# Kernel optimization log

Hardware: AMD Instinct MI355X
Metric: run time of the kernel (lower is better)

Reference implementation:

```python
import jax, jax.numpy as jnp
import numpy as np

B, S, D, H = 2, 2048, 1024, 16
DK = D // H  # 64


def setup_inputs() -> dict:
    key = jax.random.key(0)
    ks = jax.random.split(key, 11)
    std = 1.0 / np.sqrt(D)
    inp = {
        "q": jax.random.normal(ks[0], (B, S, D), jnp.float32),
        "k": jax.random.normal(ks[1], (B, S, D), jnp.float32),
        "v": jax.random.normal(ks[2], (B, S, D), jnp.float32),
        # causal mask: True means masked (matches masked_fill(mask == True, -1e9))
        "mask": jnp.triu(jnp.ones((1, 1, S, S), dtype=bool), k=1),
        "Wq": jax.random.normal(ks[3], (D, D), jnp.float32) * std,
        "bq": jnp.zeros((D,), jnp.float32),
        "Wk": jax.random.normal(ks[4], (D, D), jnp.float32) * std,
        "bk": jnp.zeros((D,), jnp.float32),
        "Wv": jax.random.normal(ks[5], (D, D), jnp.float32) * std,
        "bv": jnp.zeros((D,), jnp.float32),
        "Wo": jax.random.normal(ks[6], (D, D), jnp.float32) * std,
        "bo": jnp.zeros((D,), jnp.float32),
    }
    return inp


def _split_heads(x):
    b, s, _ = x.shape
    return x.reshape(b, s, H, DK).transpose(0, 2, 1, 3)  # [B,H,S,DK]


def reference(q, k, v, mask, Wq, bq, Wk, bk, Wv, bv, Wo, bo):
    # QKV projections (nn.Linear: x @ W.T + b)
    qh = _split_heads(q @ Wq.T + bq)
    kh = _split_heads(k @ Wk.T + bk)
    vh = _split_heads(v @ Wv.T + bv)
    # scaled dot-product attention (dropout is identity in eval)
    scores = jnp.einsum("bhqd,bhkd->bhqk", qh, kh) / jnp.sqrt(
        jnp.asarray(DK, jnp.float32))
    scores = jnp.where(mask, jnp.float32(-1e9), scores)
    attn = jax.nn.softmax(scores, axis=-1)
    out = jnp.einsum("bhqk,bhkd->bhqd", attn, vh)
    # combine heads [B,H,S,DK] -> [B,S,D], then output projection
    out = out.transpose(0, 2, 1, 3).reshape(q.shape[0], -1, D)
    return out @ Wo.T + bo
```

## Files before the change

### kernel.cpp

```cpp
#include <hip/hip_runtime.h>
#include <stdint.h>

#define S_LEN 2048
#define DMODEL 1024
#define NHEAD 16
#define DKH 64

typedef __attribute__((ext_vector_type(8))) short short8;
typedef __attribute__((ext_vector_type(4))) short sv4;
typedef __attribute__((ext_vector_type(4))) float fv4;
typedef __attribute__((ext_vector_type(8))) __bf16 bf16x8;
typedef __attribute__((ext_vector_type(4))) float f32x4;

#define QSCALE 0.18033688011112042f

static __device__ __forceinline__ short f2bf(float f) {
  unsigned u = __builtin_bit_cast(unsigned, f);
  u = u + 0x7fffu + ((u >> 16) & 1u);
  return (short)(u >> 16);
}

static __device__ __forceinline__ bf16x8 ldfrag(const void* p) {
  return __builtin_bit_cast(bf16x8, *(const short8*)p);
}

#define GLL16(gp, lp) __builtin_amdgcn_global_load_lds( \
    (const __attribute__((address_space(1))) unsigned int*)(const void*)(gp), \
    (__attribute__((address_space(3))) unsigned int*)(void*)(lp), 16, 0, 0)

#define WAIT_VMCNT0() asm volatile("s_waitcnt vmcnt(0)" ::: "memory")
#define WAIT_LGKM0()  asm volatile("s_waitcnt lgkmcnt(0)" ::: "memory")

__global__ __launch_bounds__(256) void convert_all(
    const float* __restrict__ q, const float* __restrict__ k, const float* __restrict__ v,
    const float* __restrict__ wq, const float* __restrict__ wk, const float* __restrict__ wv,
    const float* __restrict__ wo,
    short* __restrict__ xb, short* __restrict__ wb, short* __restrict__ wob)
{
  const int total = 4194304;
  for (int gid = blockIdx.x * blockDim.x + threadIdx.x; gid < total;
       gid += gridDim.x * blockDim.x) {
    const float* src; short* dst; int off; float scl = 1.0f;
    if (gid < 3145728) {
      int z = gid >> 20;
      off = (gid & 1048575) << 2;
      src = (z == 0) ? q : (z == 1) ? k : v;
      dst = xb + (size_t)z * 4194304;
    } else {
      int g = gid - 3145728;
      int z = g >> 18;
      off = (g & 262143) << 2;
      src = (z == 0) ? wq : (z == 1) ? wk : (z == 2) ? wv : wo;
      dst = (z < 3) ? (wb + (size_t)z * 1048576) : wob;
      if (z == 0) scl = QSCALE;
    }
    fv4 f = *(const fv4*)(src + off);
    sv4 o;
    o.x = f2bf(f.x * scl); o.y = f2bf(f.y * scl);
    o.z = f2bf(f.z * scl); o.w = f2bf(f.w * scl);
    *(sv4*)(dst + off) = o;
  }
}

__global__ __launch_bounds__(256) void gemm_proj(
    const short* __restrict__ Abase, const short* __restrict__ Wbase,
    const float* __restrict__ bias0, const float* __restrict__ bias1,
    const float* __restrict__ bias2, float bscl0,
    short* __restrict__ Cbf)
{
  const int Kd = 1024, Nd = 1024, Md = 4096;
  const int z = blockIdx.z;
  const short* A = Abase + (size_t)z * Md * Kd;
  const short* W = Wbase + (size_t)z * Nd * Kd;
  const float* bias = (z == 0) ? bias0 : (z == 1) ? bias1 : bias2;
  const float bscl = (z == 0) ? bscl0 : 1.0f;

  __shared__ short8 AB[2048];
  short8* As = AB;
  short8* Bs = AB + 1024;

  const int tid = threadIdx.x;
  const int w = tid >> 6, lane = tid & 63;
  const int wr = w >> 1, wc = w & 1;
  const int lhi = lane >> 4, llo = lane & 15;
  const int id = blockIdx.x + 8 * blockIdx.y;
  const int sw = (id & 7) * 32 + (id >> 3);
  const int n0 = (sw & 7) * 128, m0 = (sw >> 3) * 128;

  const f32x4 zero = {0.f, 0.f, 0.f, 0.f};
  f32x4 acc[4][4];
#pragma unroll
  for (int i = 0; i < 4; ++i)
#pragma unroll
    for (int j = 0; j < 4; ++j) acc[i][j] = zero;

  for (int kt = 0; kt < Kd / 64; ++kt) {
    const int k0 = kt * 64;
    __syncthreads();
#pragma unroll
    for (int inst = 0; inst < 4; ++inst) {
      int ib = w * 4096 + inst * 1024 + lane * 16;
      int row = ib >> 7;
      int colb = (ib & 127) ^ ((row & 7) << 4);
      int col = colb >> 1;
      GLL16(A + (size_t)(m0 + row) * Kd + k0 + col,
            (char*)As + (w * 4096 + inst * 1024));
      GLL16(W + (size_t)(n0 + row) * Kd + k0 + col,
            (char*)Bs + (w * 4096 + inst * 1024));
    }
    __syncthreads();
#pragma unroll
    for (int kk = 0; kk < 2; ++kk) {
      bf16x8 af[4], bfm[4];
#pragma unroll
      for (int t = 0; t < 4; ++t) {
        int arow = wr * 64 + t * 16 + llo;
        int abyte = ((arow << 7) + ((kk * 32 + lhi * 8) << 1)) ^ ((arow & 7) << 4);
        af[t] = ldfrag((const char*)As + abyte);
        int brow = wc * 64 + t * 16 + llo;
        int bbyte = ((brow << 7) + ((kk * 32 + lhi * 8) << 1)) ^ ((brow & 7) << 4);
        bfm[t] = ldfrag((const char*)Bs + bbyte);
      }
#pragma unroll
      for (int i = 0; i < 4; ++i)
#pragma unroll
        for (int j = 0; j < 4; ++j)
          acc[i][j] = __builtin_amdgcn_mfma_f32_16x16x32_bf16(af[i], bfm[j], acc[i][j], 0, 0, 0);
    }
  }

  short* Co = Cbf + (size_t)z * Md * Nd;
  __syncthreads();
  short* Cs = (short*)AB;
#pragma unroll
  for (int i = 0; i < 4; ++i) {
#pragma unroll
    for (int j = 0; j < 4; ++j) {
      int col = wc * 64 + j * 16 + llo;
      float bv_ = bias[n0 + col] * bscl;
#pragma unroll
      for (int r = 0; r < 4; ++r) {
        int row = wr * 64 + i * 16 + lhi * 4 + r;
        Cs[row * 128 + col] = f2bf(acc[i][j][r] + bv_);
      }
    }
  }
  __syncthreads();
#pragma unroll
  for (int s = 0; s < 8; ++s) {
    int lb = s * 4096 + tid * 16;
    short8 vL = *(const short8*)((const char*)Cs + lb);
    int row = lb >> 8;
    int colb = lb & 255;
    *(short8*)&Co[(size_t)(m0 + row) * Nd + n0 + (colb >> 1)] = vL;
  }
}

__global__ __launch_bounds__(256) void gemm_out(
    const short* __restrict__ A, const short* __restrict__ W,
    const float* __restrict__ bias, float* __restrict__ Cf)
{
  const int Kd = 1024, Nd = 1024;

  __shared__ short8 As[1024];
  __shared__ short8 Bs[512];

  const int tid = threadIdx.x;
  const int w = tid >> 6, lane = tid & 63;
  const int wr = w >> 1, wc = w & 1;
  const int lhi = lane >> 4, llo = lane & 15;
  const int id = blockIdx.x + 16 * blockIdx.y;
  const int sw = (id & 7) * 64 + (id >> 3);
  const int n0 = (sw & 15) * 64, m0 = (sw >> 4) * 128;

  const f32x4 zero = {0.f, 0.f, 0.f, 0.f};
  f32x4 acc[4][2];
#pragma unroll
  for (int i = 0; i < 4; ++i)
#pragma unroll
    for (int j = 0; j < 2; ++j) acc[i][j] = zero;

  for (int kt = 0; kt < Kd / 64; ++kt) {
    const int k0 = kt * 64;
    __syncthreads();
#pragma unroll
    for (int inst = 0; inst < 4; ++inst) {
      int ib = w * 4096 + inst * 1024 + lane * 16;
      int row = ib >> 7;
      int colb = (ib & 127) ^ ((row & 7) << 4);
      GLL16(A + (size_t)(m0 + row) * Kd + k0 + (colb >> 1),
            (char*)As + (w * 4096 + inst * 1024));
    }
#pragma unroll
    for (int inst = 0; inst < 2; ++inst) {
      int ib = w * 2048 + inst * 1024 + lane * 16;
      int row = ib >> 7;
      int colb = (ib & 127) ^ ((row & 7) << 4);
      GLL16(W + (size_t)(n0 + row) * Kd + k0 + (colb >> 1),
            (char*)Bs + (w * 2048 + inst * 1024));
    }
    __syncthreads();
#pragma unroll
    for (int kk = 0; kk < 2; ++kk) {
      bf16x8 af[4], bfm[2];
#pragma unroll
      for (int t = 0; t < 4; ++t) {
        int arow = wr * 64 + t * 16 + llo;
        int abyte = ((arow << 7) + ((kk * 32 + lhi * 8) << 1)) ^ ((arow & 7) << 4);
        af[t] = ldfrag((const char*)As + abyte);
      }
#pragma unroll
      for (int j = 0; j < 2; ++j) {
        int brow = wc * 32 + j * 16 + llo;
        int bbyte = ((brow << 7) + ((kk * 32 + lhi * 8) << 1)) ^ ((brow & 7) << 4);
        bfm[j] = ldfrag((const char*)Bs + bbyte);
      }
#pragma unroll
      for (int i = 0; i < 4; ++i)
#pragma unroll
        for (int j = 0; j < 2; ++j)
          acc[i][j] = __builtin_amdgcn_mfma_f32_16x16x32_bf16(af[i], bfm[j], acc[i][j], 0, 0, 0);
    }
  }

#pragma unroll
  for (int i = 0; i < 4; ++i) {
#pragma unroll
    for (int j = 0; j < 2; ++j) {
      int col = n0 + wc * 32 + j * 16 + llo;
      float bv_ = bias[col];
#pragma unroll
      for (int r = 0; r < 4; ++r) {
        int row = m0 + wr * 64 + i * 16 + lhi * 4 + r;
        Cf[(size_t)row * Nd + col] = acc[i][j][r] + bv_;
      }
    }
  }
}

__global__ __launch_bounds__(256) void attn_fwd(
    const short* __restrict__ Qp, const short* __restrict__ Kp,
    const short* __restrict__ Vp, short* __restrict__ Out)
{
  __shared__ short8 Ks[2][512];
  __shared__ short  Vt[64 * 72];
  __shared__ short  PsA[4][16 * 72];

  const int tid = threadIdx.x;
  const int w = tid >> 6, lane = tid & 63;
  const int lhi = lane >> 4, llo = lane & 15;

  const int id = blockIdx.x;
  const int g  = id & 255;
  const int kq = id >> 8;
  const int wv = g & 7;
  const int bh = g >> 3;
  const int qt = (kq == 0) ? 2 * wv : (kq == 1) ? 31 - 2 * wv
               : (kq == 2) ? 2 * wv + 1 : 30 - 2 * wv;
  const int nt = qt + 1;
  const int qbase = qt * 64;
  const int b = bh >> 4, h = bh & 15;
  const size_t rowbase = (size_t)b * S_LEN;
  const short* Kbase = Kp + rowbase * DMODEL + h * DKH;
  const short* Vbase = Vp + rowbase * DMODEL + h * DKH;

  short* Ps = PsA[w];
  const f32x4 zero = {0.f, 0.f, 0.f, 0.f};

  bf16x8 qf[2];
  {
    const short* qrow = Qp + (rowbase + qbase + w * 16 + llo) * DMODEL + h * DKH;
    qf[0] = ldfrag(qrow + lhi * 8);
    qf[1] = ldfrag(qrow + 32 + lhi * 8);
  }

  float mr[4], lr[4];
  f32x4 oacc[4];
#pragma unroll
  for (int r = 0; r < 4; ++r) { mr[r] = -3.0e38f; lr[r] = 0.f; }
#pragma unroll
  for (int dt = 0; dt < 4; ++dt) oacc[dt] = zero;

  const int kvs = lane, dgrp = w;

#pragma unroll
  for (int inst = 0; inst < 2; ++inst) {
    int ib = w * 2048 + inst * 1024 + lane * 16;
    int row = ib >> 7;
    int colb = (ib & 127) ^ ((row & 7) << 4);
    GLL16(Kbase + (size_t)row * DMODEL + (colb >> 1),
          (char*)&Ks[0][0] + (w * 2048 + inst * 1024));
  }
  short8 va, vb;
  va = *(const short8*)(Vbase + (size_t)kvs * DMODEL + dgrp * 16);
  vb = *(const short8*)(Vbase + (size_t)kvs * DMODEL + dgrp * 16 + 8);

  for (int t = 0; t < nt; ++t) {
    const int cur = t & 1, nxt = cur ^ 1;
    const int kvbase = t * 64;

    WAIT_VMCNT0();
#pragma unroll
    for (int j = 0; j < 8; ++j) Vt[(dgrp * 16 + j) * 72 + kvs] = va[j];
#pragma unroll
    for (int j = 0; j < 8; ++j) Vt[(dgrp * 16 + 8 + j) * 72 + kvs] = vb[j];
    if (t + 1 < nt) {
      const int nb = kvbase + 64;
#pragma unroll
      for (int inst = 0; inst < 2; ++inst) {
        int ib = w * 2048 + inst * 1024 + lane * 16;
        int row = ib >> 7;
        int colb = (ib & 127) ^ ((row & 7) << 4);
        GLL16(Kbase + (size_t)(nb + row) * DMODEL + (colb >> 1),
              (char*)&Ks[nxt][0] + (w * 2048 + inst * 1024));
      }
      va = *(const short8*)(Vbase + (size_t)(nb + kvs) * DMODEL + dgrp * 16);
      vb = *(const short8*)(Vbase + (size_t)(nb + kvs) * DMODEL + dgrp * 16 + 8);
    }
    WAIT_LGKM0();
    __builtin_amdgcn_s_barrier();

    f32x4 sc[4];
#pragma unroll
    for (int tt = 0; tt < 4; ++tt) sc[tt] = zero;
    __builtin_amdgcn_s_setprio(1);
#pragma unroll
    for (int kk = 0; kk < 2; ++kk) {
#pragma unroll
      for (int tt = 0; tt < 4; ++tt) {
        int krow = tt * 16 + llo;
        int kbyte = ((krow << 7) + ((kk * 32 + lhi * 8) << 1)) ^ ((krow & 7) << 4);
        bf16x8 kf = ldfrag((const char*)&Ks[cur][0] + kbyte);
        sc[tt] = __builtin_amdgcn_mfma_f32_16x16x32_bf16(qf[kk], kf, sc[tt], 0, 0, 0);
      }
    }
    __builtin_amdgcn_s_setprio(0);

    const bool diag = (t == qt);
    float sv[4][4], tmx[4];
#pragma unroll
    for (int r = 0; r < 4; ++r) {
#pragma unroll
      for (int tt = 0; tt < 4; ++tt) {
        float s = sc[tt][r];
        if (diag) {
          int kg = kvbase + tt * 16 + llo;
          int qg = qbase + w * 16 + lhi * 4 + r;
          if (kg > qg) s = -3.0e38f;
        }
        sv[tt][r] = s;
      }
      float trm = fmaxf(fmaxf(sv[0][r], sv[1][r]), fmaxf(sv[2][r], sv[3][r]));
      trm = fmaxf(trm, __shfl_xor(trm, 1));
      trm = fmaxf(trm, __shfl_xor(trm, 2));
      trm = fmaxf(trm, __shfl_xor(trm, 4));
      trm = fmaxf(trm, __shfl_xor(trm, 8));
      tmx[r] = trm;
    }
    bool grow = (tmx[0] > mr[0] + 8.f) || (tmx[1] > mr[1] + 8.f) ||
                (tmx[2] > mr[2] + 8.f) || (tmx[3] > mr[3] + 8.f);
    if (__ballot(grow)) {
#pragma unroll
      for (int r = 0; r < 4; ++r) {
        float mnew = fmaxf(mr[r], tmx[r]);
        float alpha = __builtin_amdgcn_exp2f(mr[r] - mnew);
        mr[r] = mnew;
        lr[r] *= alpha;
#pragma unroll
        for (int dt = 0; dt < 4; ++dt) oacc[dt][r] = oacc[dt][r] * alpha;
      }
    }
#pragma unroll
    for (int r = 0; r < 4; ++r) {
      float rs = 0.f;
#pragma unroll
      for (int tt = 0; tt < 4; ++tt) {
        float pv = __builtin_amdgcn_exp2f(sv[tt][r] - mr[r]);
        rs += pv;
        Ps[(lhi * 4 + r) * 72 + tt * 16 + llo] = f2bf(pv);
      }
      lr[r] += rs;
    }

    __builtin_amdgcn_s_setprio(1);
#pragma unroll
    for (int kk = 0; kk < 2; ++kk) {
      bf16x8 pa = ldfrag(Ps + llo * 72 + kk * 32 + lhi * 8);
#pragma unroll
      for (int dt = 0; dt < 4; ++dt) {
        bf16x8 vf = ldfrag(&Vt[(dt * 16 + llo) * 72 + kk * 32 + lhi * 8]);
        oacc[dt] = __builtin_amdgcn_mfma_f32_16x16x32_bf16(pa, vf, oacc[dt], 0, 0, 0);
      }
    }
    __builtin_amdgcn_s_setprio(0);
    __builtin_amdgcn_s_barrier();
  }

#pragma unroll
  for (int r = 0; r < 4; ++r) {
    float rs = lr[r];
    rs += __shfl_xor(rs, 1);
    rs += __shfl_xor(rs, 2);
    rs += __shfl_xor(rs, 4);
    rs += __shfl_xor(rs, 8);
    lr[r] = rs;
  }
#pragma unroll
  for (int dt = 0; dt < 4; ++dt) {
#pragma unroll
    for (int r = 0; r < 4; ++r) {
      float vv = oacc[dt][r] / lr[r];
      int row = qbase + w * 16 + lhi * 4 + r;
      int col = h * DKH + dt * 16 + llo;
      Out[(rowbase + row) * DMODEL + col] = f2bf(vv);
    }
  }
}

extern "C" void kernel_launch(void* const* d_in, const int* in_sizes, int n_in,
                              void* d_out, int out_size, void* d_ws, size_t ws_size,
                              hipStream_t stream) {
  (void)in_sizes; (void)n_in; (void)out_size; (void)ws_size;
  const float* q  = (const float*)d_in[0];
  const float* k  = (const float*)d_in[1];
  const float* v  = (const float*)d_in[2];
  const float* Wq = (const float*)d_in[4];
  const float* bq = (const float*)d_in[5];
  const float* Wk = (const float*)d_in[6];
  const float* bk = (const float*)d_in[7];
  const float* Wv = (const float*)d_in[8];
  const float* bv = (const float*)d_in[9];
  const float* Wo = (const float*)d_in[10];
  const float* bo = (const float*)d_in[11];
  float* out = (float*)d_out;

  short* xb   = (short*)d_ws;
  short* wb   = xb + 3ull * 4194304;
  short* wob  = wb + 3ull * 1048576;
  short* proj = wob + 1048576;
  short* attno = xb;

  convert_all<<<dim3(2048), dim3(256), 0, stream>>>(q, k, v, Wq, Wk, Wv, Wo, xb, wb, wob);
  gemm_proj<<<dim3(8, 32, 3), dim3(256), 0, stream>>>(xb, wb, bq, bk, bv, QSCALE, proj);
  attn_fwd<<<dim3(1024), dim3(256), 0, stream>>>(proj, proj + 4194304ull,
                                                 proj + 2ull * 4194304, attno);
  gemm_out<<<dim3(16, 32), dim3(256), 0, stream>>>(attno, wob, bo, out);
}
```

Baseline: 256.4 us.

## Double-buffer GEMM LDS tiles and widen attention blocks to 128 query rows

Both projection GEMMs now stage the next K-tile into a second LDS buffer with global_load_lds before computing on the current one. Partial vmcnt waits and s_barrier replace the two __syncthreads per iteration, so loads overlap the MFMA work at the cost of doubled LDS use. The attention kernel moves to 512-thread blocks covering 128 query rows (8 waves), which halves the grid and shares each K/V tile between twice as many query rows. This adds per-block work imbalance and a wider diagonal-masking range.

New measurement: 257.3 us. Within noise of the previous version (+0.3%).

```diff
diff --git a/kernel.cpp b/kernel.cpp
--- a/kernel.cpp
+++ b/kernel.cpp
@@ -28,7 +28,7 @@
     (const __attribute__((address_space(1))) unsigned int*)(const void*)(gp), \
     (__attribute__((address_space(3))) unsigned int*)(void*)(lp), 16, 0, 0)
 
-#define WAIT_VMCNT0() asm volatile("s_waitcnt vmcnt(0)" ::: "memory")
+#define WAIT_VMCNT(N) asm volatile("s_waitcnt vmcnt(" #N ")" ::: "memory")
 #define WAIT_LGKM0()  asm volatile("s_waitcnt lgkmcnt(0)" ::: "memory")
 
 __global__ __launch_bounds__(256) void convert_all(
@@ -75,9 +75,7 @@
   const float* bias = (z == 0) ? bias0 : (z == 1) ? bias1 : bias2;
   const float bscl = (z == 0) ? bscl0 : 1.0f;
 
-  __shared__ short8 AB[2048];
-  short8* As = AB;
-  short8* Bs = AB + 1024;
+  __shared__ short8 AB[4096];
 
   const int tid = threadIdx.x;
   const int w = tid >> 6, lane = tid & 63;
@@ -94,9 +92,7 @@
 #pragma unroll
     for (int j = 0; j < 4; ++j) acc[i][j] = zero;
 
-  for (int kt = 0; kt < Kd / 64; ++kt) {
-    const int k0 = kt * 64;
-    __syncthreads();
+  auto stage = [&](int buf, int k0) {
 #pragma unroll
     for (int inst = 0; inst < 4; ++inst) {
       int ib = w * 4096 + inst * 1024 + lane * 16;
@@ -104,11 +100,24 @@
       int colb = (ib & 127) ^ ((row & 7) << 4);
       int col = colb >> 1;
       GLL16(A + (size_t)(m0 + row) * Kd + k0 + col,
-            (char*)As + (w * 4096 + inst * 1024));
+            (char*)AB + buf * 32768 + (w * 4096 + inst * 1024));
       GLL16(W + (size_t)(n0 + row) * Kd + k0 + col,
-            (char*)Bs + (w * 4096 + inst * 1024));
-    }
-    __syncthreads();
+            (char*)AB + buf * 32768 + 16384 + (w * 4096 + inst * 1024));
+    }
+  };
+
+  stage(0, 0);
+  for (int kt = 0; kt < 16; ++kt) {
+    const int cur = kt & 1, nxt = cur ^ 1;
+    if (kt < 15) {
+      stage(nxt, (kt + 1) * 64);
+      WAIT_VMCNT(8);
+    } else {
+      WAIT_VMCNT(0);
+    }
+    __builtin_amdgcn_s_barrier();
+    const char* As = (const char*)AB + cur * 32768;
+    const char* Bs = As + 16384;
 #pragma unroll
     for (int kk = 0; kk < 2; ++kk) {
       bf16x8 af[4], bfm[4];
@@ -116,10 +125,10 @@
       for (int t = 0; t < 4; ++t) {
         int arow = wr * 64 + t * 16 + llo;
         int abyte = ((arow << 7) + ((kk * 32 + lhi * 8) << 1)) ^ ((arow & 7) << 4);
-        af[t] = ldfrag((const char*)As + abyte);
+        af[t] = ldfrag(As + abyte);
         int brow = wc * 64 + t * 16 + llo;
         int bbyte = ((brow << 7) + ((kk * 32 + lhi * 8) << 1)) ^ ((brow & 7) << 4);
-        bfm[t] = ldfrag((const char*)Bs + bbyte);
+        bfm[t] = ldfrag(Bs + bbyte);
       }
 #pragma unroll
       for (int i = 0; i < 4; ++i)
@@ -127,6 +136,7 @@
         for (int j = 0; j < 4; ++j)
           acc[i][j] = __builtin_amdgcn_mfma_f32_16x16x32_bf16(af[i], bfm[j], acc[i][j], 0, 0, 0);
     }
+    __builtin_amdgcn_s_barrier();
   }
 
   short* Co = Cbf + (size_t)z * Md * Nd;
@@ -162,8 +172,7 @@
 {
   const int Kd = 1024, Nd = 1024;
 
-  __shared__ short8 As[1024];
-  __shared__ short8 Bs[512];
+  __shared__ short8 AB[3072];
 
   const int tid = threadIdx.x;
   const int w = tid >> 6, lane = tid & 63;
@@ -180,16 +189,14 @@
 #pragma unroll
     for (int j = 0; j < 2; ++j) acc[i][j] = zero;
 
-  for (int kt = 0; kt < Kd / 64; ++kt) {
-    const int k0 = kt * 64;
-    __syncthreads();
+  auto stage = [&](int buf, int k0) {
 #pragma unroll
     for (int inst = 0; inst < 4; ++inst) {
       int ib = w * 4096 + inst * 1024 + lane * 16;
       int row = ib >> 7;
       int colb = (ib & 127) ^ ((row & 7) << 4);
       GLL16(A + (size_t)(m0 + row) * Kd + k0 + (colb >> 1),
-            (char*)As + (w * 4096 + inst * 1024));
+            (char*)AB + buf * 24576 + (w * 4096 + inst * 1024));
     }
 #pragma unroll
     for (int inst = 0; inst < 2; ++inst) {
@@ -197,9 +204,22 @@
       int row = ib >> 7;
       int colb = (ib & 127) ^ ((row & 7) << 4);
       GLL16(W + (size_t)(n0 + row) * Kd + k0 + (colb >> 1),
-            (char*)Bs + (w * 2048 + inst * 1024));
-    }
-    __syncthreads();
+            (char*)AB + buf * 24576 + 16384 + (w * 2048 + inst * 1024));
+    }
+  };
+
+  stage(0, 0);
+  for (int kt = 0; kt < 16; ++kt) {
+    const int cur = kt & 1, nxt = cur ^ 1;
+    if (kt < 15) {
+      stage(nxt, (kt + 1) * 64);
+      WAIT_VMCNT(6);
+    } else {
+      WAIT_VMCNT(0);
+    }
+    __builtin_amdgcn_s_barrier();
+    const char* As = (const char*)AB + cur * 24576;
+    const char* Bs = As + 16384;
 #pragma unroll
     for (int kk = 0; kk < 2; ++kk) {
       bf16x8 af[4], bfm[2];
@@ -207,13 +227,13 @@
       for (int t = 0; t < 4; ++t) {
         int arow = wr * 64 + t * 16 + llo;
         int abyte = ((arow << 7) + ((kk * 32 + lhi * 8) << 1)) ^ ((arow & 7) << 4);
-        af[t] = ldfrag((const char*)As + abyte);
+        af[t] = ldfrag(As + abyte);
       }
 #pragma unroll
       for (int j = 0; j < 2; ++j) {
         int brow = wc * 32 + j * 16 + llo;
         int bbyte = ((brow << 7) + ((kk * 32 + lhi * 8) << 1)) ^ ((brow & 7) << 4);
-        bfm[j] = ldfrag((const char*)Bs + bbyte);
+        bfm[j] = ldfrag(Bs + bbyte);
       }
 #pragma unroll
       for (int i = 0; i < 4; ++i)
@@ -221,6 +241,7 @@
         for (int j = 0; j < 2; ++j)
           acc[i][j] = __builtin_amdgcn_mfma_f32_16x16x32_bf16(af[i], bfm[j], acc[i][j], 0, 0, 0);
     }
+    __builtin_amdgcn_s_barrier();
   }
 
 #pragma unroll
@@ -238,27 +259,26 @@
   }
 }
 
-__global__ __launch_bounds__(256) void attn_fwd(
+__global__ __launch_bounds__(512) void attn_fwd(
     const short* __restrict__ Qp, const short* __restrict__ Kp,
     const short* __restrict__ Vp, short* __restrict__ Out)
 {
   __shared__ short8 Ks[2][512];
   __shared__ short  Vt[64 * 72];
-  __shared__ short  PsA[4][16 * 72];
+  __shared__ short  PsA[8][16 * 72];
 
   const int tid = threadIdx.x;
   const int w = tid >> 6, lane = tid & 63;
   const int lhi = lane >> 4, llo = lane & 15;
 
   const int id = blockIdx.x;
-  const int g  = id & 255;
-  const int kq = id >> 8;
+  const int half = id >> 8;
+  const int g = id & 255;
+  const int bh = g >> 3;
   const int wv = g & 7;
-  const int bh = g >> 3;
-  const int qt = (kq == 0) ? 2 * wv : (kq == 1) ? 31 - 2 * wv
-               : (kq == 2) ? 2 * wv + 1 : 30 - 2 * wv;
-  const int nt = qt + 1;
-  const int qbase = qt * 64;
+  const int qt = half ? (15 - 2 * wv) : (2 * wv);
+  const int nt = 2 * qt + 2;
+  const int qbase = qt * 128;
   const int b = bh >> 4, h = bh & 15;
   const size_t rowbase = (size_t)b * S_LEN;
   const short* Kbase = Kp + rowbase * DMODEL + h * DKH;
@@ -281,41 +301,31 @@
 #pragma unroll
   for (int dt = 0; dt < 4; ++dt) oacc[dt] = zero;
 
-  const int kvs = lane, dgrp = w;
-
-#pragma unroll
-  for (int inst = 0; inst < 2; ++inst) {
-    int ib = w * 2048 + inst * 1024 + lane * 16;
+  const int kvs = lane;
+
+  {
+    int ib = tid * 16;
     int row = ib >> 7;
     int colb = (ib & 127) ^ ((row & 7) << 4);
-    GLL16(Kbase + (size_t)row * DMODEL + (colb >> 1),
-          (char*)&Ks[0][0] + (w * 2048 + inst * 1024));
-  }
-  short8 va, vb;
-  va = *(const short8*)(Vbase + (size_t)kvs * DMODEL + dgrp * 16);
-  vb = *(const short8*)(Vbase + (size_t)kvs * DMODEL + dgrp * 16 + 8);
+    GLL16(Kbase + (size_t)row * DMODEL + (colb >> 1), (char*)&Ks[0][0] + ib);
+  }
+  short8 va = *(const short8*)(Vbase + (size_t)kvs * DMODEL + w * 8);
 
   for (int t = 0; t < nt; ++t) {
     const int cur = t & 1, nxt = cur ^ 1;
     const int kvbase = t * 64;
 
-    WAIT_VMCNT0();
-#pragma unroll
-    for (int j = 0; j < 8; ++j) Vt[(dgrp * 16 + j) * 72 + kvs] = va[j];
-#pragma unroll
-    for (int j = 0; j < 8; ++j) Vt[(dgrp * 16 + 8 + j) * 72 + kvs] = vb[j];
+    asm volatile("s_waitcnt vmcnt(0)" ::: "memory");
+#pragma unroll
+    for (int j = 0; j < 8; ++j) Vt[(w * 8 + j) * 72 + kvs] = va[j];
     if (t + 1 < nt) {
       const int nb = kvbase + 64;
-#pragma unroll
-      for (int inst = 0; inst < 2; ++inst) {
-        int ib = w * 2048 + inst * 1024 + lane * 16;
-        int row = ib >> 7;
-        int colb = (ib & 127) ^ ((row & 7) << 4);
-        GLL16(Kbase + (size_t)(nb + row) * DMODEL + (colb >> 1),
-              (char*)&Ks[nxt][0] + (w * 2048 + inst * 1024));
-      }
-      va = *(const short8*)(Vbase + (size_t)(nb + kvs) * DMODEL + dgrp * 16);
-      vb = *(const short8*)(Vbase + (size_t)(nb + kvs) * DMODEL + dgrp * 16 + 8);
+      int ib = tid * 16;
+      int row = ib >> 7;
+      int colb = (ib & 127) ^ ((row & 7) << 4);
+      GLL16(Kbase + (size_t)(nb + row) * DMODEL + (colb >> 1),
+            (char*)&Ks[nxt][0] + ib);
+      va = *(const short8*)(Vbase + (size_t)(nb + kvs) * DMODEL + w * 8);
     }
     WAIT_LGKM0();
     __builtin_amdgcn_s_barrier();
@@ -336,7 +346,7 @@
     }
     __builtin_amdgcn_s_setprio(0);
 
-    const bool diag = (t == qt);
+    const bool diag = (t >= nt - 2);
     float sv[4][4], tmx[4];
 #pragma unroll
     for (int r = 0; r < 4; ++r) {
@@ -442,7 +452,7 @@
 
   convert_all<<<dim3(2048), dim3(256), 0, stream>>>(q, k, v, Wq, Wk, Wv, Wo, xb, wb, wob);
   gemm_proj<<<dim3(8, 32, 3), dim3(256), 0, stream>>>(xb, wb, bq, bk, bv, QSCALE, proj);
-  attn_fwd<<<dim3(1024), dim3(256), 0, stream>>>(proj, proj + 4194304ull,
-                                                 proj + 2ull * 4194304, attno);
+  attn_fwd<<<dim3(512), dim3(512), 0, stream>>>(proj, proj + 4194304ull,
+                                                proj + 2ull * 4194304, attno);
   gemm_out<<<dim3(16, 32), dim3(256), 0, stream>>>(attno, wob, bo, out);
 }
```
